# Performance work log

Hardware: AMD Instinct MI355X
Metric: run time of the kernel (lower is better)

Reference implementation:

```python
import jax, jax.numpy as jnp
import numpy as np

N_NODES = 50000
N_EDGES = 800000
HID = 128
EDGE_DIM = 4
LAYERS = 4
MAX_Z = 100
NUM_GRAPHS = 512


def setup_inputs() -> dict:
    key = jax.random.key(0)
    ks = jax.random.split(key, 16)
    s = lambda k, shape, fan_in: jax.random.normal(k, shape, jnp.float32) / np.sqrt(fan_in)
    inp = {
        "z": jax.random.randint(ks[0], (N_NODES,), 0, MAX_Z + 1),
        "edge_index": jax.random.randint(ks[1], (2, N_EDGES), 0, N_NODES),
        "edge_attr": jax.random.normal(ks[2], (N_EDGES, EDGE_DIM), jnp.float32),
        "batch": jnp.sort(jax.random.randint(ks[3], (N_NODES,), 0, NUM_GRAPHS)),
        "emb": jax.random.normal(ks[4], (MAX_Z + 1, HID), jnp.float32),
        # stacked per-layer params; Linear stored as [in, out]
        "ew1": s(ks[5], (LAYERS, 2 * HID + EDGE_DIM, HID), 2 * HID + EDGE_DIM),
        "eb1": jnp.zeros((LAYERS, HID), jnp.float32),
        "ew2": s(ks[6], (LAYERS, HID, HID), HID),
        "eb2": jnp.zeros((LAYERS, HID), jnp.float32),
        "nw": s(ks[7], (LAYERS, 2 * HID, HID), 2 * HID),
        "nb": jnp.zeros((LAYERS, HID), jnp.float32),
        "rw1": s(ks[8], (HID, HID), HID),
        "rb1": jnp.zeros((HID,), jnp.float32),
        "rw2": s(ks[9], (HID, 1), HID),
        "rb2": jnp.zeros((1,), jnp.float32),
    }
    return inp


def _forward(z, edge_index, edge_attr, batch,
             emb, ew1, eb1, ew2, eb2, nw, nb, rw1, rb1, rw2, rb2):
    silu = jax.nn.silu
    src, dst = edge_index[0], edge_index[1]
    x = emb[z]  # [N, H]
    for l in range(LAYERS):
        m_in = jnp.concatenate([x[src], x[dst], edge_attr], axis=-1)  # [E, 2H+ed]
        h = silu(m_in @ ew1[l] + eb1[l])
        msg = silu(h @ ew2[l] + eb2[l])  # [E, H]
        agg = jax.ops.segment_sum(msg, dst, num_segments=N_NODES)  # scatter-add
        x = silu(jnp.concatenate([x, agg], axis=-1) @ nw[l] + nb[l])
    # segment mean over graphs
    sums = jax.ops.segment_sum(x, batch, num_segments=NUM_GRAPHS)
    counts = jnp.clip(jax.ops.segment_sum(jnp.ones((x.shape[0],), x.dtype), batch,
                                          num_segments=NUM_GRAPHS), 1.0)[:, None]
    g = sums / counts  # [G, H]
    pred = (silu(g @ rw1 + rb1) @ rw2 + rb2)[:, 0]  # [G]
    return pred


def reference(z, edge_index, edge_attr, batch,
              emb, ew1, eb1, ew2, eb2, nw, nb, rw1, rb1, rw2, rb2):
    return _forward(z, edge_index, edge_attr, batch,
                    emb, ew1, eb1, ew2, eb2, nw, nb, rw1, rb1, rw2, rb2)
```

## Files before the change

kernel.cpp:

```cpp
#include <hip/hip_runtime.h>
#include <math.h>

#define HID  128
#define EDIM 4

typedef unsigned short u16;
typedef u16    us8   __attribute__((ext_vector_type(8)));
typedef __bf16 bf16x8 __attribute__((ext_vector_type(8)));
typedef float  f32x4 __attribute__((ext_vector_type(4)));

__device__ __forceinline__ float silu_f(float v) {
    return v * __builtin_amdgcn_rcpf(1.0f + __expf(-v));
}
__device__ __forceinline__ u16 f2bf(float f) {
    unsigned u = __float_as_uint(f);
    unsigned r = u + 0x7fffu + ((u >> 16) & 1u);
    return (u16)(r >> 16);
}
__device__ __forceinline__ u16 f2bf_fast(float f) {
    return (u16)((__float_as_uint(f) + 0x8000u) >> 16);
}
__device__ __forceinline__ unsigned pack_bf2(float a, float b) {
    return ((__float_as_uint(a) + 0x8000u) >> 16) |
           ((__float_as_uint(b) + 0x8000u) & 0xffff0000u);
}
__device__ __forceinline__ float bf2f(u16 s) {
    return __uint_as_float(((unsigned)s) << 16);
}
__device__ __forceinline__ bf16x8 as_bf(us8 v) {
    return __builtin_bit_cast(bf16x8, v);
}

__device__ __forceinline__ void wfrag_gen(const float* __restrict__ w,
        u16* __restrict__ out, int KT, int Kdata, int Kstride,
        int split, int jump, int idx) {
    int lane = idx & 63;
    int f    = (idx >> 6) % (KT * 8);
    int l    = idx / (64 * KT * 8);
    int kt = f >> 3, nt = f & 7;
    int n  = nt * 16 + (lane & 15);
    int k0 = kt * 32 + ((lane >> 4) * 8);
    us8 v;
    #pragma unroll
    for (int j = 0; j < 8; ++j) {
        int k = k0 + j;
        int row = k + (k >= split ? jump : 0);
        v[j] = (row < Kdata) ? f2bf(w[((size_t)l * Kstride + row) * HID + n]) : (u16)0;
    }
    *(us8*)&out[((size_t)(l * KT * 8 + f) * 64 + lane) * 8] = v;
}

#define T1A (4 * 5 * 8 * 64)
#define T1B (4 * 4 * 8 * 64)
#define T2  (4 * 4 * 8 * 64)
#define T3  (4 * 8 * 8 * 64)

__global__ __launch_bounds__(256) void setup_kernel(
        const float* __restrict__ ew1, const float* __restrict__ ew2,
        const float* __restrict__ nw,
        u16* __restrict__ w1af, u16* __restrict__ w1bf,
        u16* __restrict__ w2f, u16* __restrict__ nwf,
        int* __restrict__ cnt, int* __restrict__ cursor,
        float* __restrict__ sums, float* __restrict__ cnts_g, int N, int G) {
    const int BIG = 1 << 30;
    int idx = blockIdx.x * 256 + threadIdx.x;
    if (idx < T1A) { wfrag_gen(ew1, w1af, 5, 260, 260, 128, 128, idx); return; }
    idx -= T1A;
    if (idx < T1B) { wfrag_gen(ew1, w1bf, 4, 260, 260, 0, 128, idx); return; }
    idx -= T1B;
    if (idx < T2) { wfrag_gen(ew2, w2f, 4, 128, 128, BIG, 0, idx); return; }
    idx -= T2;
    if (idx < T3) { wfrag_gen(nw, nwf, 8, 256, 256, BIG, 0, idx); return; }
    idx -= T3;
    if (idx < N) { cnt[idx] = 0; return; }
    idx -= N;
    if (idx < N) { cursor[idx] = 0; return; }
    idx -= N;
    if (idx < G * HID) { sums[idx] = 0.f; return; }
    idx -= G * HID;
    if (idx < G) { cnts_g[idx] = 0.f; return; }
}

__global__ __launch_bounds__(256) void hist_kernel(const int* __restrict__ dst,
        int* __restrict__ cnt, int E) {
    int e = blockIdx.x * 256 + threadIdx.x;
    if (e < E) atomicAdd(&cnt[dst[e]], 1);
}

__global__ __launch_bounds__(1024) void scan_kernel(const int* __restrict__ cnt,
        int* __restrict__ rowptr, int n) {
    __shared__ int s[1024];
    const int t = threadIdx.x;
    const int chunk = (n + 1023) >> 10;
    int lo = t * chunk, hi = lo + chunk;
    if (lo > n) lo = n;
    if (hi > n) hi = n;
    int sum = 0;
    for (int i = lo; i < hi; ++i) sum += cnt[i];
    s[t] = sum;
    __syncthreads();
    for (int off = 1; off < 1024; off <<= 1) {
        int v = (t >= off) ? s[t - off] : 0;
        __syncthreads();
        s[t] += v;
        __syncthreads();
    }
    int run = s[t] - sum;
    for (int i = lo; i < hi; ++i) { rowptr[i] = run; run += cnt[i]; }
    if (t == 1023) rowptr[n] = run;
}

__global__ __launch_bounds__(256) void scatter_kernel(const int* __restrict__ src,
        const int* __restrict__ dst, const float* __restrict__ ea,
        const int* __restrict__ rowptr, int* __restrict__ cursor,
        int* __restrict__ srcS, int* __restrict__ dstS, u16* __restrict__ eaS, int E) {
    int e = blockIdx.x * 256 + threadIdx.x;
    if (e >= E) return;
    int d = dst[e];
    int p = rowptr[d] + atomicAdd(&cursor[d], 1);
    srcS[p] = src[e];
    dstS[p] = d;
    const float* q = &ea[(size_t)e * EDIM];
    ushort4 v;
    v.x = f2bf(q[0]); v.y = f2bf(q[1]); v.z = f2bf(q[2]); v.w = f2bf(q[3]);
    *(ushort4*)&eaS[(size_t)p * 4] = v;
}

__global__ __launch_bounds__(HID) void embed_kernel(const int* __restrict__ z,
        const float* __restrict__ emb, u16* __restrict__ xb,
        float* __restrict__ agg, const int* __restrict__ batch,
        float* __restrict__ counts, int n) {
    int i = blockIdx.x;
    if (i >= n) return;
    int t = threadIdx.x;
    xb[(size_t)i * HID + t] = f2bf(emb[(size_t)z[i] * HID + t]);
    agg[(size_t)i * HID + t] = 0.f;
    if (t == 0) unsafeAtomicAdd(&counts[batch[i]], 1.0f);
}

__global__ __launch_bounds__(256) void y_kernel(
        const u16* __restrict__ xb, const u16* __restrict__ w1bf,
        float* __restrict__ Y, int n) {
    const int t    = threadIdx.x;
    const int i0   = blockIdx.x * 32;
    const int wv   = t >> 6, lane = t & 63;
    const int lrow = lane & 15;
    const int kq   = lane >> 4;
    const int kq8  = kq * 8;

    int iN[2];
    #pragma unroll
    for (int mt = 0; mt < 2; ++mt) {
        int i = i0 + mt * 16 + lrow; if (i >= n) i = n - 1;
        iN[mt] = i;
    }
    f32x4 acc[2][2];
    #pragma unroll
    for (int mt = 0; mt < 2; ++mt)
        #pragma unroll
        for (int nt = 0; nt < 2; ++nt)
            acc[mt][nt] = (f32x4){0.f, 0.f, 0.f, 0.f};

    #pragma unroll
    for (int kt = 0; kt < 4; ++kt) {
        bf16x8 w0 = *(const bf16x8*)&w1bf[((size_t)(kt * 8 + wv * 2 + 0) * 64 + lane) * 8];
        bf16x8 w1 = *(const bf16x8*)&w1bf[((size_t)(kt * 8 + wv * 2 + 1) * 64 + lane) * 8];
        #pragma unroll
        for (int mt = 0; mt < 2; ++mt) {
            bf16x8 a = as_bf(*(const us8*)&xb[(size_t)iN[mt] * HID + kt * 32 + kq8]);
            acc[mt][0] = __builtin_amdgcn_mfma_f32_16x16x32_bf16(w0, a, acc[mt][0], 0, 0, 0);
            acc[mt][1] = __builtin_amdgcn_mfma_f32_16x16x32_bf16(w1, a, acc[mt][1], 0, 0, 0);
        }
    }
    #pragma unroll
    for (int mt = 0; mt < 2; ++mt) {
        int node = i0 + mt * 16 + lrow;
        if (node < n) {
            #pragma unroll
            for (int nt = 0; nt < 2; ++nt)
                *(f32x4*)&Y[(size_t)node * HID + (wv * 2 + nt) * 16 + kq * 4] = acc[mt][nt];
        }
    }
}

__global__ __launch_bounds__(512, 8) void edge_mfma(
        const u16* __restrict__ xin, const int* __restrict__ srcS,
        const int* __restrict__ dstS, const u16* __restrict__ eaS,
        const u16* __restrict__ w1af, const float* __restrict__ b1,
        const u16* __restrict__ w2f, const float* __restrict__ b2,
        const float* __restrict__ Y,
        float* __restrict__ agg, int nE) {
    __shared__ __align__(16) char smem[64 * 132 * 4];
    __shared__ __align__(16) int dsh[64];
    u16*   A = (u16*)smem;
    u16*   H = (u16*)smem;
    float* M = (float*)smem;

    const int t    = threadIdx.x;
    const int e0   = blockIdx.x * 64;
    const int wv   = t >> 6, lane = t & 63;
    const int lrow = lane & 15;
    const int kq   = lane >> 4;
    const int kq8  = kq * 8;
    const int rq   = kq * 4;
    const int h    = wv >> 2;
    const int p    = wv & 3;

    #pragma unroll
    for (int it = 0; it < 2; ++it) {
        int slot = it * 512 + t;
        int row = slot >> 4, ch = slot & 15;
        int e = e0 + row; if (e >= nE) e = nE - 1;
        int node = srcS[e];
        us8 v = *(const us8*)&xin[(size_t)node * HID + ch * 8];
        *(us8*)&A[row * 168 + ch * 8] = v;
    }
    if (t < 64) {
        int e = e0 + t;
        bool valid = e < nE; if (!valid) e = nE - 1;
        dsh[t] = valid ? dstS[e] : -1;
        ushort4 q = *(const ushort4*)&eaS[(size_t)e * 4];
        int base = t * 168 + 128;
        us8 z8 = (us8){0, 0, 0, 0, 0, 0, 0, 0};
        *(us8*)&A[base + 8]  = z8;
        *(us8*)&A[base + 16] = z8;
        *(us8*)&A[base + 24] = z8;
        A[base + 0] = q.x; A[base + 1] = q.y; A[base + 2] = q.z; A[base + 3] = q.w;
        A[base + 4] = 0;   A[base + 5] = 0;   A[base + 6] = 0;   A[base + 7] = 0;
    }
    __syncthreads();

    f32x4 acc[2][2];
    #pragma unroll
    for (int mt = 0; mt < 2; ++mt) {
        int edge = (h * 2 + mt) * 16 + lrow;
        int d = dsh[edge]; if (d < 0) d = 0;
        #pragma unroll
        for (int nt = 0; nt < 2; ++nt) {
            f32x4 bv = *(const f32x4*)&b1[(p * 2 + nt) * 16 + rq];
            f32x4 yv = *(const f32x4*)&Y[(size_t)d * HID + (p * 2 + nt) * 16 + rq];
            acc[mt][nt] = bv + yv;
        }
    }
    #pragma unroll
    for (int kt = 0; kt < 5; ++kt) {
        bf16x8 w0 = *(const bf16x8*)&w1af[((size_t)(kt * 8 + p * 2 + 0) * 64 + lane) * 8];
        bf16x8 w1 = *(const bf16x8*)&w1af[((size_t)(kt * 8 + p * 2 + 1) * 64 + lane) * 8];
        #pragma unroll
        for (int mt = 0; mt < 2; ++mt) {
            bf16x8 a = *(const bf16x8*)&A[((h * 2 + mt) * 16 + lrow) * 168 + kt * 32 + kq8];
            acc[mt][0] = __builtin_amdgcn_mfma_f32_16x16x32_bf16(w0, a, acc[mt][0], 0, 0, 0);
            acc[mt][1] = __builtin_amdgcn_mfma_f32_16x16x32_bf16(w1, a, acc[mt][1], 0, 0, 0);
        }
    }
    __syncthreads();

    #pragma unroll
    for (int mt = 0; mt < 2; ++mt)
        #pragma unroll
        for (int nt = 0; nt < 2; ++nt) {
            uint2 hv;
            hv.x = pack_bf2(silu_f(acc[mt][nt][0]), silu_f(acc[mt][nt][1]));
            hv.y = pack_bf2(silu_f(acc[mt][nt][2]), silu_f(acc[mt][nt][3]));
            int edge = (h * 2 + mt) * 16 + lrow;
            *(uint2*)&H[edge * 136 + (p * 2 + nt) * 16 + rq] = hv;
        }
    __syncthreads();

    f32x4 acc2[2][2];
    #pragma unroll
    for (int nt = 0; nt < 2; ++nt) {
        f32x4 bv = *(const f32x4*)&b2[(p * 2 + nt) * 16 + rq];
        acc2[0][nt] = bv; acc2[1][nt] = bv;
    }
    #pragma unroll
    for (int kt = 0; kt < 4; ++kt) {
        bf16x8 w0 = *(const bf16x8*)&w2f[((size_t)(kt * 8 + p * 2 + 0) * 64 + lane) * 8];
        bf16x8 w1 = *(const bf16x8*)&w2f[((size_t)(kt * 8 + p * 2 + 1) * 64 + lane) * 8];
        #pragma unroll
        for (int mt = 0; mt < 2; ++mt) {
            bf16x8 a = *(const bf16x8*)&H[((h * 2 + mt) * 16 + lrow) * 136 + kt * 32 + kq8];
            acc2[mt][0] = __builtin_amdgcn_mfma_f32_16x16x32_bf16(w0, a, acc2[mt][0], 0, 0, 0);
            acc2[mt][1] = __builtin_amdgcn_mfma_f32_16x16x32_bf16(w1, a, acc2[mt][1], 0, 0, 0);
        }
    }
    __syncthreads();

    #pragma unroll
    for (int mt = 0; mt < 2; ++mt)
        #pragma unroll
        for (int nt = 0; nt < 2; ++nt) {
            f32x4 mv;
            #pragma unroll
            for (int r = 0; r < 4; ++r) mv[r] = silu_f(acc2[mt][nt][r]);
            int edge = (h * 2 + mt) * 16 + lrow;
            *(f32x4*)&M[edge * 132 + (p * 2 + nt) * 16 + rq] = mv;
        }

    {
        int col = p * 32 + (lane & 31);
        int r0  = h * 32 + (lane >> 5) * 16;
        int4 da = *(const int4*)&dsh[r0];
        int4 db = *(const int4*)&dsh[r0 + 4];
        int4 dc = *(const int4*)&dsh[r0 + 8];
        int4 dd = *(const int4*)&dsh[r0 + 12];
        int ds_[16] = {da.x, da.y, da.z, da.w, db.x, db.y, db.z, db.w,
                       dc.x, dc.y, dc.z, dc.w, dd.x, dd.y, dd.z, dd.w};
        float run = 0.f;
        int   cur = ds_[0];
        #pragma unroll
        for (int i = 0; i < 16; ++i) {
            run += M[(r0 + i) * 132 + col];
            int nxt = (i == 15) ? -2 : ds_[i + 1];
            if (cur != nxt) {
                if (cur >= 0)
                    unsafeAtomicAdd(&agg[(size_t)cur * HID + col], run);
                run = 0.f; cur = nxt;
            }
        }
    }
}

__global__ __launch_bounds__(256) void node_mfma(
        u16* __restrict__ xb, float* __restrict__ agg,
        const u16* __restrict__ nwf, const float* __restrict__ nb,
        const int* __restrict__ batch, float* __restrict__ sums,
        int last, int n) {
    const int t    = threadIdx.x;
    const int i0   = blockIdx.x * 32;
    const int wv   = t >> 6, lane = t & 63;
    const int lrow = lane & 15;
    const int kq   = lane >> 4;
    const int kq8  = kq * 8;
    const int rq   = kq * 4;

    int iN[2];
    #pragma unroll
    for (int mt = 0; mt < 2; ++mt) {
        int i = i0 + mt * 16 + lrow; if (i >= n) i = n - 1;
        iN[mt] = i;
    }

    f32x4 acc[2][2];
    {
        float bias0 = nb[wv * 32 + lrow], bias1 = nb[wv * 32 + 16 + lrow];
        #pragma unroll
        for (int mt = 0; mt < 2; ++mt)
            #pragma unroll
            for (int r = 0; r < 4; ++r) {
                acc[mt][0][r] = bias0; acc[mt][1][r] = bias1;
            }
    }
    #pragma unroll
    for (int kt = 0; kt < 4; ++kt) {
        bf16x8 w0 = *(const bf16x8*)&nwf[((size_t)(kt * 8 + wv * 2 + 0) * 64 + lane) * 8];
        bf16x8 w1 = *(const bf16x8*)&nwf[((size_t)(kt * 8 + wv * 2 + 1) * 64 + lane) * 8];
        #pragma unroll
        for (int mt = 0; mt < 2; ++mt) {
            bf16x8 a = as_bf(*(const us8*)&xb[(size_t)iN[mt] * HID + kt * 32 + kq8]);
            acc[mt][0] = __builtin_amdgcn_mfma_f32_16x16x32_bf16(a, w0, acc[mt][0], 0, 0, 0);
            acc[mt][1] = __builtin_amdgcn_mfma_f32_16x16x32_bf16(a, w1, acc[mt][1], 0, 0, 0);
        }
    }
    #pragma unroll
    for (int kt = 4; kt < 8; ++kt) {
        bf16x8 w0 = *(const bf16x8*)&nwf[((size_t)(kt * 8 + wv * 2 + 0) * 64 + lane) * 8];
        bf16x8 w1 = *(const bf16x8*)&nwf[((size_t)(kt * 8 + wv * 2 + 1) * 64 + lane) * 8];
        #pragma unroll
        for (int mt = 0; mt < 2; ++mt) {
            const float* pa = &agg[(size_t)iN[mt] * HID + (kt - 4) * 32 + kq8];
            float4 f0 = *(const float4*)pa;
            float4 f1 = *(const float4*)(pa + 4);
            us8 av;
            av[0] = f2bf_fast(f0.x); av[1] = f2bf_fast(f0.y);
            av[2] = f2bf_fast(f0.z); av[3] = f2bf_fast(f0.w);
            av[4] = f2bf_fast(f1.x); av[5] = f2bf_fast(f1.y);
            av[6] = f2bf_fast(f1.z); av[7] = f2bf_fast(f1.w);
            bf16x8 a = as_bf(av);
            acc[mt][0] = __builtin_amdgcn_mfma_f32_16x16x32_bf16(a, w0, acc[mt][0], 0, 0, 0);
            acc[mt][1] = __builtin_amdgcn_mfma_f32_16x16x32_bf16(a, w1, acc[mt][1], 0, 0, 0);
        }
    }

    if (!last) {
        __syncthreads();
        const float4 z4 = make_float4(0.f, 0.f, 0.f, 0.f);
        #pragma unroll
        for (int kt = 0; kt < 4; ++kt)
            #pragma unroll
            for (int mt = 0; mt < 2; ++mt) {
                float* pa = &agg[(size_t)iN[mt] * HID + kt * 32 + kq8];
                *(float4*)pa = z4; *(float4*)(pa + 4) = z4;
            }
        #pragma unroll
        for (int mt = 0; mt < 2; ++mt)
            #pragma unroll
            for (int nt2 = 0; nt2 < 2; ++nt2)
                #pragma unroll
                for (int r = 0; r < 4; ++r) {
                    int i = i0 + mt * 16 + rq + r;
                    if (i < n)
                        xb[(size_t)i * HID + wv * 32 + nt2 * 16 + lrow] =
                            f2bf_fast(silu_f(acc[mt][nt2][r]));
                }
    } else {
        #pragma unroll
        for (int mt = 0; mt < 2; ++mt)
            #pragma unroll
            for (int nt2 = 0; nt2 < 2; ++nt2)
                #pragma unroll
                for (int r = 0; r < 4; ++r) {
                    int i = i0 + mt * 16 + rq + r;
                    if (i < n) {
                        int b = batch[i];
                        unsafeAtomicAdd(&sums[(size_t)b * HID + wv * 32 + nt2 * 16 + lrow],
                                        silu_f(acc[mt][nt2][r]));
                    }
                }
    }
}

__global__ __launch_bounds__(HID) void readout_kernel(
        const float* __restrict__ sums, const float* __restrict__ counts,
        const float* __restrict__ rw1, const float* __restrict__ rb1,
        const float* __restrict__ rw2, const float* __restrict__ rb2,
        float* __restrict__ pred) {
    __shared__ float gv[HID];
    __shared__ float hv[HID];
    const int g = blockIdx.x;
    const int t = threadIdx.x;
    float c = counts[g];
    if (c < 1.0f) c = 1.0f;
    gv[t] = sums[(size_t)g * HID + t] / c;
    __syncthreads();
    float acc = rb1[t];
    for (int k4 = 0; k4 < 32; ++k4) {
        float4 mv = *(const float4*)&gv[k4 * 4];
        #pragma unroll
        for (int j = 0; j < 4; ++j)
            acc += ((const float*)&mv)[j] * rw1[(size_t)(k4 * 4 + j) * HID + t];
    }
    hv[t] = silu_f(acc) * rw2[t];
    __syncthreads();
    for (int s = HID / 2; s > 0; s >>= 1) {
        if (t < s) hv[t] += hv[t + s];
        __syncthreads();
    }
    if (t == 0) pred[g] = hv[0] + rb2[0];
}

extern "C" void kernel_launch(void* const* d_in, const int* in_sizes, int n_in,
                              void* d_out, int out_size, void* d_ws, size_t ws_size,
                              hipStream_t stream) {
    const int*   z          = (const int*)d_in[0];
    const int*   edge_index = (const int*)d_in[1];
    const float* edge_attr  = (const float*)d_in[2];
    const int*   batch      = (const int*)d_in[3];
    const float* emb        = (const float*)d_in[4];
    const float* ew1        = (const float*)d_in[5];
    const float* eb1        = (const float*)d_in[6];
    const float* ew2        = (const float*)d_in[7];
    const float* eb2        = (const float*)d_in[8];
    const float* nw         = (const float*)d_in[9];
    const float* nb         = (const float*)d_in[10];
    const float* rw1        = (const float*)d_in[11];
    const float* rb1        = (const float*)d_in[12];
    const float* rw2        = (const float*)d_in[13];
    const float* rb2        = (const float*)d_in[14];
    float* pred = (float*)d_out;

    const int N = in_sizes[0];
    const int E = in_sizes[1] / 2;
    const int G = out_size;
    const int* srcI = edge_index;
    const int* dstI = edge_index + E;

    char* base = (char*)d_ws;
    size_t off = 0;
    auto carve = [&](size_t bytes) -> char* {
        char* p = base + off;
        off = (off + bytes + 255) & ~(size_t)255;
        return p;
    };
    float* agg    = (float*)carve((size_t)N * HID * sizeof(float));
    float* sums   = (float*)carve((size_t)G * HID * sizeof(float));
    float* cnts_g = (float*)carve((size_t)G * sizeof(float));
    u16*   xb     = (u16*)carve((size_t)N * HID * sizeof(u16));
    float* Y      = (float*)carve((size_t)N * HID * sizeof(float));
    int*   srcS   = (int*)carve((size_t)(E + 64) * sizeof(int));
    int*   dstS   = (int*)carve((size_t)(E + 64) * sizeof(int));
    u16*   eaS    = (u16*)carve((size_t)(E + 64) * 4 * sizeof(u16));
    int*   rowptr = (int*)carve((size_t)(N + 1) * sizeof(int));
    int*   cursor = (int*)carve((size_t)N * sizeof(int));
    int*   cnt    = (int*)carve((size_t)N * sizeof(int));
    u16*   w1af   = (u16*)carve((size_t)4 * 40 * 512 * sizeof(u16));
    u16*   w1bf   = (u16*)carve((size_t)4 * 32 * 512 * sizeof(u16));
    u16*   w2f    = (u16*)carve((size_t)4 * 32 * 512 * sizeof(u16));
    u16*   nwf    = (u16*)carve((size_t)4 * 64 * 512 * sizeof(u16));

    {
        long long total = (long long)T1A + T1B + T2 + T3 + 2LL * N + (long long)G * HID + G;
        int blocks = (int)((total + 255) / 256);
        setup_kernel<<<blocks, 256, 0, stream>>>(ew1, ew2, nw, w1af, w1bf, w2f, nwf,
                                                 cnt, cursor, sums, cnts_g, N, G);
    }

    hist_kernel<<<(E + 255) / 256, 256, 0, stream>>>(dstI, cnt, E);
    scan_kernel<<<1, 1024, 0, stream>>>(cnt, rowptr, N);
    scatter_kernel<<<(E + 255) / 256, 256, 0, stream>>>(
        srcI, dstI, edge_attr, rowptr, cursor, srcS, dstS, eaS, E);

    embed_kernel<<<N, HID, 0, stream>>>(z, emb, xb, agg, batch, cnts_g, N);

    for (int l = 0; l < 4; ++l) {
        y_kernel<<<(N + 31) / 32, 256, 0, stream>>>(
            xb, w1bf + (size_t)l * 32 * 512, Y, N);
        edge_mfma<<<(E + 63) / 64, 512, 0, stream>>>(
            xb, srcS, dstS, eaS,
            w1af + (size_t)l * 40 * 512, eb1 + (size_t)l * HID,
            w2f + (size_t)l * 32 * 512, eb2 + (size_t)l * HID,
            Y, agg, E);
        node_mfma<<<(N + 31) / 32, 256, 0, stream>>>(
            xb, agg, nwf + (size_t)l * 64 * 512, nb + (size_t)l * HID,
            batch, sums, (l == 3) ? 1 : 0, N);
    }

    readout_kernel<<<G, HID, 0, stream>>>(sums, cnts_g, rw1, rb1, rw2, rb2, pred);
}
```

Baseline: 1.127 ms.

## Fuse edge, node and next-layer projection into one dst-partitioned kernel

Each layer now runs as a single kernel in which every block owns 32 destination nodes. The block walks that node range's CSR edge tiles and sums messages into shared memory (aggL), so the global fp32 agg buffer, its zeroing and its global atomics are gone. After the edge tiles, the same block runs the node update and the next layer's Y projection, with x ping-ponged between two buffers. The cost is far fewer blocks, each doing a variable number of serial tiles, which can cause load imbalance. The extra shared memory may also lower occupancy.

```diff
diff --git a/kernel.cpp b/kernel.cpp
--- a/kernel.cpp
+++ b/kernel.cpp
@@ -128,13 +128,11 @@
 
 __global__ __launch_bounds__(HID) void embed_kernel(const int* __restrict__ z,
         const float* __restrict__ emb, u16* __restrict__ xb,
-        float* __restrict__ agg, const int* __restrict__ batch,
-        float* __restrict__ counts, int n) {
+        const int* __restrict__ batch, float* __restrict__ counts, int n) {
     int i = blockIdx.x;
     if (i >= n) return;
     int t = threadIdx.x;
     xb[(size_t)i * HID + t] = f2bf(emb[(size_t)z[i] * HID + t]);
-    agg[(size_t)i * HID + t] = 0.f;
     if (t == 0) unsafeAtomicAdd(&counts[batch[i]], 1.0f);
 }
 
@@ -183,21 +181,25 @@
     }
 }
 
-__global__ __launch_bounds__(512, 8) void edge_mfma(
-        const u16* __restrict__ xin, const int* __restrict__ srcS,
-        const int* __restrict__ dstS, const u16* __restrict__ eaS,
+__global__ __launch_bounds__(512, 6) void fused_layer(
+        const u16* __restrict__ xin, u16* __restrict__ xout,
+        const int* __restrict__ srcS, const int* __restrict__ dstS,
+        const u16* __restrict__ eaS, const int* __restrict__ rowptr,
         const u16* __restrict__ w1af, const float* __restrict__ b1,
         const u16* __restrict__ w2f, const float* __restrict__ b2,
-        const float* __restrict__ Y,
-        float* __restrict__ agg, int nE) {
+        float* __restrict__ Y, const u16* __restrict__ w1bf_nxt,
+        const u16* __restrict__ nwf, const float* __restrict__ nb,
+        const int* __restrict__ batch, float* __restrict__ sums,
+        int last, int N) {
     __shared__ __align__(16) char smem[64 * 132 * 4];
     __shared__ __align__(16) int dsh[64];
-    u16*   A = (u16*)smem;
-    u16*   H = (u16*)smem;
-    float* M = (float*)smem;
+    __shared__ __align__(16) float aggL[32 * HID];
+    u16*   A   = (u16*)smem;
+    u16*   H   = (u16*)smem;
+    float* M   = (float*)smem;
+    u16*   xnS = (u16*)smem;
 
     const int t    = threadIdx.x;
-    const int e0   = blockIdx.x * 64;
     const int wv   = t >> 6, lane = t & 63;
     const int lrow = lane & 15;
     const int kq   = lane >> 4;
@@ -206,217 +208,210 @@
     const int h    = wv >> 2;
     const int p    = wv & 3;
 
-    #pragma unroll
-    for (int it = 0; it < 2; ++it) {
-        int slot = it * 512 + t;
-        int row = slot >> 4, ch = slot & 15;
-        int e = e0 + row; if (e >= nE) e = nE - 1;
-        int node = srcS[e];
-        us8 v = *(const us8*)&xin[(size_t)node * HID + ch * 8];
-        *(us8*)&A[row * 168 + ch * 8] = v;
-    }
-    if (t < 64) {
-        int e = e0 + t;
-        bool valid = e < nE; if (!valid) e = nE - 1;
-        dsh[t] = valid ? dstS[e] : -1;
-        ushort4 q = *(const ushort4*)&eaS[(size_t)e * 4];
-        int base = t * 168 + 128;
-        us8 z8 = (us8){0, 0, 0, 0, 0, 0, 0, 0};
-        *(us8*)&A[base + 8]  = z8;
-        *(us8*)&A[base + 16] = z8;
-        *(us8*)&A[base + 24] = z8;
-        A[base + 0] = q.x; A[base + 1] = q.y; A[base + 2] = q.z; A[base + 3] = q.w;
-        A[base + 4] = 0;   A[base + 5] = 0;   A[base + 6] = 0;   A[base + 7] = 0;
+    const int n0  = blockIdx.x * 32;
+    int nhi = n0 + 32; if (nhi > N) nhi = N;
+    const int rs = rowptr[n0];
+    const int re = rowptr[nhi];
+    const int ntiles = (re - rs + 63) >> 6;
+
+    #pragma unroll
+    for (int i = 0; i < 2; ++i)
+        ((f32x4*)aggL)[i * 512 + t] = (f32x4){0.f, 0.f, 0.f, 0.f};
+
+    for (int tile = 0; tile < ntiles; ++tile) {
+        const int e0 = rs + tile * 64;
+        __syncthreads();
+
+        #pragma unroll
+        for (int it = 0; it < 2; ++it) {
+            int slot = it * 512 + t;
+            int row = slot >> 4, ch = slot & 15;
+            int e = e0 + row; if (e >= re) e = re - 1;
+            int node = srcS[e];
+            us8 v = *(const us8*)&xin[(size_t)node * HID + ch * 8];
+            *(us8*)&A[row * 168 + ch * 8] = v;
+        }
+        if (t < 64) {
+            int e = e0 + t;
+            bool valid = e < re; if (!valid) e = re - 1;
+            dsh[t] = valid ? (dstS[e] - n0) : -1;
+            ushort4 q = *(const ushort4*)&eaS[(size_t)e * 4];
+            int base = t * 168 + 128;
+            us8 z8 = (us8){0, 0, 0, 0, 0, 0, 0, 0};
+            *(us8*)&A[base + 8]  = z8;
+            *(us8*)&A[base + 16] = z8;
+            *(us8*)&A[base + 24] = z8;
+            A[base + 0] = q.x; A[base + 1] = q.y; A[base + 2] = q.z; A[base + 3] = q.w;
+            A[base + 4] = 0;   A[base + 5] = 0;   A[base + 6] = 0;   A[base + 7] = 0;
+        }
+        __syncthreads();
+
+        f32x4 acc[2][2];
+        #pragma unroll
+        for (int mt = 0; mt < 2; ++mt) {
+            int edge = (h * 2 + mt) * 16 + lrow;
+            int d = dsh[edge]; if (d < 0) d = 0;
+            #pragma unroll
+            for (int nt = 0; nt < 2; ++nt) {
+                f32x4 bv = *(const f32x4*)&b1[(p * 2 + nt) * 16 + rq];
+                f32x4 yv = *(const f32x4*)&Y[(size_t)(n0 + d) * HID + (p * 2 + nt) * 16 + rq];
+                acc[mt][nt] = bv + yv;
+            }
+        }
+        #pragma unroll
+        for (int kt = 0; kt < 5; ++kt) {
+            bf16x8 w0 = *(const bf16x8*)&w1af[((size_t)(kt * 8 + p * 2 + 0) * 64 + lane) * 8];
+            bf16x8 w1 = *(const bf16x8*)&w1af[((size_t)(kt * 8 + p * 2 + 1) * 64 + lane) * 8];
+            #pragma unroll
+            for (int mt = 0; mt < 2; ++mt) {
+                bf16x8 a = *(const bf16x8*)&A[((h * 2 + mt) * 16 + lrow) * 168 + kt * 32 + kq8];
+                acc[mt][0] = __builtin_amdgcn_mfma_f32_16x16x32_bf16(w0, a, acc[mt][0], 0, 0, 0);
+                acc[mt][1] = __builtin_amdgcn_mfma_f32_16x16x32_bf16(w1, a, acc[mt][1], 0, 0, 0);
+            }
+        }
+        __syncthreads();
+
+        #pragma unroll
+        for (int mt = 0; mt < 2; ++mt)
+            #pragma unroll
+            for (int nt = 0; nt < 2; ++nt) {
+                uint2 hv;
+                hv.x = pack_bf2(silu_f(acc[mt][nt][0]), silu_f(acc[mt][nt][1]));
+                hv.y = pack_bf2(silu_f(acc[mt][nt][2]), silu_f(acc[mt][nt][3]));
+                int edge = (h * 2 + mt) * 16 + lrow;
+                *(uint2*)&H[edge * 136 + (p * 2 + nt) * 16 + rq] = hv;
+            }
+        __syncthreads();
+
+        f32x4 acc2[2][2];
+        #pragma unroll
+        for (int nt = 0; nt < 2; ++nt) {
+            f32x4 bv = *(const f32x4*)&b2[(p * 2 + nt) * 16 + rq];
+            acc2[0][nt] = bv; acc2[1][nt] = bv;
+        }
+        #pragma unroll
+        for (int kt = 0; kt < 4; ++kt) {
+            bf16x8 w0 = *(const bf16x8*)&w2f[((size_t)(kt * 8 + p * 2 + 0) * 64 + lane) * 8];
+            bf16x8 w1 = *(const bf16x8*)&w2f[((size_t)(kt * 8 + p * 2 + 1) * 64 + lane) * 8];
+            #pragma unroll
+            for (int mt = 0; mt < 2; ++mt) {
+                bf16x8 a = *(const bf16x8*)&H[((h * 2 + mt) * 16 + lrow) * 136 + kt * 32 + kq8];
+                acc2[mt][0] = __builtin_amdgcn_mfma_f32_16x16x32_bf16(w0, a, acc2[mt][0], 0, 0, 0);
+                acc2[mt][1] = __builtin_amdgcn_mfma_f32_16x16x32_bf16(w1, a, acc2[mt][1], 0, 0, 0);
+            }
+        }
+        __syncthreads();
+
+        #pragma unroll
+        for (int mt = 0; mt < 2; ++mt)
+            #pragma unroll
+            for (int nt = 0; nt < 2; ++nt) {
+                f32x4 mv;
+                #pragma unroll
+                for (int r = 0; r < 4; ++r) mv[r] = silu_f(acc2[mt][nt][r]);
+                int edge = (h * 2 + mt) * 16 + lrow;
+                *(f32x4*)&M[edge * 132 + (p * 2 + nt) * 16 + rq] = mv;
+            }
+
+        {
+            int col = p * 32 + (lane & 31);
+            int r0  = h * 32 + (lane >> 5) * 16;
+            int4 da = *(const int4*)&dsh[r0];
+            int4 db = *(const int4*)&dsh[r0 + 4];
+            int4 dc = *(const int4*)&dsh[r0 + 8];
+            int4 dd = *(const int4*)&dsh[r0 + 12];
+            int ds_[16] = {da.x, da.y, da.z, da.w, db.x, db.y, db.z, db.w,
+                           dc.x, dc.y, dc.z, dc.w, dd.x, dd.y, dd.z, dd.w};
+            float run = 0.f;
+            int   cur = ds_[0];
+            #pragma unroll
+            for (int i = 0; i < 16; ++i) {
+                run += M[(r0 + i) * 132 + col];
+                int nxt = (i == 15) ? -2 : ds_[i + 1];
+                if (cur != nxt) {
+                    if (cur >= 0)
+                        atomicAdd(&aggL[cur * HID + col], run);
+                    run = 0.f; cur = nxt;
+                }
+            }
+        }
     }
     __syncthreads();
 
-    f32x4 acc[2][2];
-    #pragma unroll
-    for (int mt = 0; mt < 2; ++mt) {
-        int edge = (h * 2 + mt) * 16 + lrow;
-        int d = dsh[edge]; if (d < 0) d = 0;
-        #pragma unroll
-        for (int nt = 0; nt < 2; ++nt) {
-            f32x4 bv = *(const f32x4*)&b1[(p * 2 + nt) * 16 + rq];
-            f32x4 yv = *(const f32x4*)&Y[(size_t)d * HID + (p * 2 + nt) * 16 + rq];
-            acc[mt][nt] = bv + yv;
-        }
-    }
-    #pragma unroll
-    for (int kt = 0; kt < 5; ++kt) {
-        bf16x8 w0 = *(const bf16x8*)&w1af[((size_t)(kt * 8 + p * 2 + 0) * 64 + lane) * 8];
-        bf16x8 w1 = *(const bf16x8*)&w1af[((size_t)(kt * 8 + p * 2 + 1) * 64 + lane) * 8];
-        #pragma unroll
-        for (int mt = 0; mt < 2; ++mt) {
-            bf16x8 a = *(const bf16x8*)&A[((h * 2 + mt) * 16 + lrow) * 168 + kt * 32 + kq8];
-            acc[mt][0] = __builtin_amdgcn_mfma_f32_16x16x32_bf16(w0, a, acc[mt][0], 0, 0, 0);
-            acc[mt][1] = __builtin_amdgcn_mfma_f32_16x16x32_bf16(w1, a, acc[mt][1], 0, 0, 0);
-        }
-    }
-    __syncthreads();
-
+    f32x4 accN[2];
     #pragma unroll
     for (int mt = 0; mt < 2; ++mt)
-        #pragma unroll
-        for (int nt = 0; nt < 2; ++nt) {
-            uint2 hv;
-            hv.x = pack_bf2(silu_f(acc[mt][nt][0]), silu_f(acc[mt][nt][1]));
-            hv.y = pack_bf2(silu_f(acc[mt][nt][2]), silu_f(acc[mt][nt][3]));
-            int edge = (h * 2 + mt) * 16 + lrow;
-            *(uint2*)&H[edge * 136 + (p * 2 + nt) * 16 + rq] = hv;
-        }
-    __syncthreads();
-
-    f32x4 acc2[2][2];
-    #pragma unroll
-    for (int nt = 0; nt < 2; ++nt) {
-        f32x4 bv = *(const f32x4*)&b2[(p * 2 + nt) * 16 + rq];
-        acc2[0][nt] = bv; acc2[1][nt] = bv;
-    }
+        accN[mt] = *(const f32x4*)&nb[wv * 16 + rq];
     #pragma unroll
     for (int kt = 0; kt < 4; ++kt) {
-        bf16x8 w0 = *(const bf16x8*)&w2f[((size_t)(kt * 8 + p * 2 + 0) * 64 + lane) * 8];
-        bf16x8 w1 = *(const bf16x8*)&w2f[((size_t)(kt * 8 + p * 2 + 1) * 64 + lane) * 8];
-        #pragma unroll
-        for (int mt = 0; mt < 2; ++mt) {
-            bf16x8 a = *(const bf16x8*)&H[((h * 2 + mt) * 16 + lrow) * 136 + kt * 32 + kq8];
-            acc2[mt][0] = __builtin_amdgcn_mfma_f32_16x16x32_bf16(w0, a, acc2[mt][0], 0, 0, 0);
-            acc2[mt][1] = __builtin_amdgcn_mfma_f32_16x16x32_bf16(w1, a, acc2[mt][1], 0, 0, 0);
-        }
-    }
-    __syncthreads();
-
-    #pragma unroll
-    for (int mt = 0; mt < 2; ++mt)
-        #pragma unroll
-        for (int nt = 0; nt < 2; ++nt) {
-            f32x4 mv;
-            #pragma unroll
-            for (int r = 0; r < 4; ++r) mv[r] = silu_f(acc2[mt][nt][r]);
-            int edge = (h * 2 + mt) * 16 + lrow;
-            *(f32x4*)&M[edge * 132 + (p * 2 + nt) * 16 + rq] = mv;
-        }
-
-    {
-        int col = p * 32 + (lane & 31);
-        int r0  = h * 32 + (lane >> 5) * 16;
-        int4 da = *(const int4*)&dsh[r0];
-        int4 db = *(const int4*)&dsh[r0 + 4];
-        int4 dc = *(const int4*)&dsh[r0 + 8];
-        int4 dd = *(const int4*)&dsh[r0 + 12];
-        int ds_[16] = {da.x, da.y, da.z, da.w, db.x, db.y, db.z, db.w,
-                       dc.x, dc.y, dc.z, dc.w, dd.x, dd.y, dd.z, dd.w};
-        float run = 0.f;
-        int   cur = ds_[0];
-        #pragma unroll
-        for (int i = 0; i < 16; ++i) {
-            run += M[(r0 + i) * 132 + col];
-            int nxt = (i == 15) ? -2 : ds_[i + 1];
-            if (cur != nxt) {
-                if (cur >= 0)
-                    unsafeAtomicAdd(&agg[(size_t)cur * HID + col], run);
-                run = 0.f; cur = nxt;
-            }
-        }
-    }
-}
-
-__global__ __launch_bounds__(256) void node_mfma(
-        u16* __restrict__ xb, float* __restrict__ agg,
-        const u16* __restrict__ nwf, const float* __restrict__ nb,
-        const int* __restrict__ batch, float* __restrict__ sums,
-        int last, int n) {
-    const int t    = threadIdx.x;
-    const int i0   = blockIdx.x * 32;
-    const int wv   = t >> 6, lane = t & 63;
-    const int lrow = lane & 15;
-    const int kq   = lane >> 4;
-    const int kq8  = kq * 8;
-    const int rq   = kq * 4;
-
-    int iN[2];
-    #pragma unroll
-    for (int mt = 0; mt < 2; ++mt) {
-        int i = i0 + mt * 16 + lrow; if (i >= n) i = n - 1;
-        iN[mt] = i;
-    }
-
-    f32x4 acc[2][2];
-    {
-        float bias0 = nb[wv * 32 + lrow], bias1 = nb[wv * 32 + 16 + lrow];
-        #pragma unroll
-        for (int mt = 0; mt < 2; ++mt)
-            #pragma unroll
-            for (int r = 0; r < 4; ++r) {
-                acc[mt][0][r] = bias0; acc[mt][1][r] = bias1;
-            }
-    }
-    #pragma unroll
-    for (int kt = 0; kt < 4; ++kt) {
-        bf16x8 w0 = *(const bf16x8*)&nwf[((size_t)(kt * 8 + wv * 2 + 0) * 64 + lane) * 8];
-        bf16x8 w1 = *(const bf16x8*)&nwf[((size_t)(kt * 8 + wv * 2 + 1) * 64 + lane) * 8];
-        #pragma unroll
-        for (int mt = 0; mt < 2; ++mt) {
-            bf16x8 a = as_bf(*(const us8*)&xb[(size_t)iN[mt] * HID + kt * 32 + kq8]);
-            acc[mt][0] = __builtin_amdgcn_mfma_f32_16x16x32_bf16(a, w0, acc[mt][0], 0, 0, 0);
-            acc[mt][1] = __builtin_amdgcn_mfma_f32_16x16x32_bf16(a, w1, acc[mt][1], 0, 0, 0);
+        bf16x8 w = *(const bf16x8*)&nwf[((size_t)(kt * 8 + wv) * 64 + lane) * 8];
+        #pragma unroll
+        for (int mt = 0; mt < 2; ++mt) {
+            int nd = n0 + mt * 16 + lrow; if (nd >= N) nd = N - 1;
+            bf16x8 a = as_bf(*(const us8*)&xin[(size_t)nd * HID + kt * 32 + kq8]);
+            accN[mt] = __builtin_amdgcn_mfma_f32_16x16x32_bf16(w, a, accN[mt], 0, 0, 0);
         }
     }
     #pragma unroll
     for (int kt = 4; kt < 8; ++kt) {
-        bf16x8 w0 = *(const bf16x8*)&nwf[((size_t)(kt * 8 + wv * 2 + 0) * 64 + lane) * 8];
-        bf16x8 w1 = *(const bf16x8*)&nwf[((size_t)(kt * 8 + wv * 2 + 1) * 64 + lane) * 8];
-        #pragma unroll
-        for (int mt = 0; mt < 2; ++mt) {
-            const float* pa = &agg[(size_t)iN[mt] * HID + (kt - 4) * 32 + kq8];
-            float4 f0 = *(const float4*)pa;
-            float4 f1 = *(const float4*)(pa + 4);
+        bf16x8 w = *(const bf16x8*)&nwf[((size_t)(kt * 8 + wv) * 64 + lane) * 8];
+        #pragma unroll
+        for (int mt = 0; mt < 2; ++mt) {
+            const float* pa = &aggL[(mt * 16 + lrow) * HID + (kt - 4) * 32 + kq8];
+            f32x4 f0 = *(const f32x4*)pa;
+            f32x4 f1 = *(const f32x4*)(pa + 4);
             us8 av;
-            av[0] = f2bf_fast(f0.x); av[1] = f2bf_fast(f0.y);
-            av[2] = f2bf_fast(f0.z); av[3] = f2bf_fast(f0.w);
-            av[4] = f2bf_fast(f1.x); av[5] = f2bf_fast(f1.y);
-            av[6] = f2bf_fast(f1.z); av[7] = f2bf_fast(f1.w);
-            bf16x8 a = as_bf(av);
-            acc[mt][0] = __builtin_amdgcn_mfma_f32_16x16x32_bf16(a, w0, acc[mt][0], 0, 0, 0);
-            acc[mt][1] = __builtin_amdgcn_mfma_f32_16x16x32_bf16(a, w1, acc[mt][1], 0, 0, 0);
+            av[0] = f2bf_fast(f0[0]); av[1] = f2bf_fast(f0[1]);
+            av[2] = f2bf_fast(f0[2]); av[3] = f2bf_fast(f0[3]);
+            av[4] = f2bf_fast(f1[0]); av[5] = f2bf_fast(f1[1]);
+            av[6] = f2bf_fast(f1[2]); av[7] = f2bf_fast(f1[3]);
+            accN[mt] = __builtin_amdgcn_mfma_f32_16x16x32_bf16(w, as_bf(av), accN[mt], 0, 0, 0);
         }
     }
 
     if (!last) {
-        __syncthreads();
-        const float4 z4 = make_float4(0.f, 0.f, 0.f, 0.f);
-        #pragma unroll
-        for (int kt = 0; kt < 4; ++kt)
+        #pragma unroll
+        for (int mt = 0; mt < 2; ++mt) {
+            uint2 xv;
+            xv.x = pack_bf2(silu_f(accN[mt][0]), silu_f(accN[mt][1]));
+            xv.y = pack_bf2(silu_f(accN[mt][2]), silu_f(accN[mt][3]));
+            int node = mt * 16 + lrow;
+            *(uint2*)&xnS[node * HID + wv * 16 + rq] = xv;
+            if (n0 + node < N)
+                *(uint2*)&xout[(size_t)(n0 + node) * HID + wv * 16 + rq] = xv;
+        }
+        __syncthreads();
+
+        f32x4 accY[2];
+        accY[0] = (f32x4){0.f, 0.f, 0.f, 0.f};
+        accY[1] = (f32x4){0.f, 0.f, 0.f, 0.f};
+        #pragma unroll
+        for (int kt = 0; kt < 4; ++kt) {
+            bf16x8 w = *(const bf16x8*)&w1bf_nxt[((size_t)(kt * 8 + wv) * 64 + lane) * 8];
             #pragma unroll
             for (int mt = 0; mt < 2; ++mt) {
-                float* pa = &agg[(size_t)iN[mt] * HID + kt * 32 + kq8];
-                *(float4*)pa = z4; *(float4*)(pa + 4) = z4;
-            }
-        #pragma unroll
-        for (int mt = 0; mt < 2; ++mt)
-            #pragma unroll
-            for (int nt2 = 0; nt2 < 2; ++nt2)
+                bf16x8 a = as_bf(*(const us8*)&xnS[(mt * 16 + lrow) * HID + kt * 32 + kq8]);
+                accY[mt] = __builtin_amdgcn_mfma_f32_16x16x32_bf16(w, a, accY[mt], 0, 0, 0);
+            }
+        }
+        #pragma unroll
+        for (int mt = 0; mt < 2; ++mt) {
+            int node = mt * 16 + lrow;
+            if (n0 + node < N)
+                *(f32x4*)&Y[(size_t)(n0 + node) * HID + wv * 16 + rq] = accY[mt];
+        }
+    } else {
+        #pragma unroll
+        for (int mt = 0; mt < 2; ++mt) {
+            int node = mt * 16 + lrow;
+            if (n0 + node < N) {
+                int b = batch[n0 + node];
                 #pragma unroll
-                for (int r = 0; r < 4; ++r) {
-                    int i = i0 + mt * 16 + rq + r;
-                    if (i < n)
-                        xb[(size_t)i * HID + wv * 32 + nt2 * 16 + lrow] =
-                            f2bf_fast(silu_f(acc[mt][nt2][r]));
-                }
-    } else {
-        #pragma unroll
-        for (int mt = 0; mt < 2; ++mt)
-            #pragma unroll
-            for (int nt2 = 0; nt2 < 2; ++nt2)
-                #pragma unroll
-                for (int r = 0; r < 4; ++r) {
-                    int i = i0 + mt * 16 + rq + r;
-                    if (i < n) {
-                        int b = batch[i];
-                        unsafeAtomicAdd(&sums[(size_t)b * HID + wv * 32 + nt2 * 16 + lrow],
-                                        silu_f(acc[mt][nt2][r]));
-                    }
-                }
+                for (int r = 0; r < 4; ++r)
+                    unsafeAtomicAdd(&sums[(size_t)b * HID + wv * 16 + rq + r],
+                                    silu_f(accN[mt][r]));
+            }
+        }
     }
 }
 
@@ -482,10 +477,10 @@
         off = (off + bytes + 255) & ~(size_t)255;
         return p;
     };
-    float* agg    = (float*)carve((size_t)N * HID * sizeof(float));
     float* sums   = (float*)carve((size_t)G * HID * sizeof(float));
     float* cnts_g = (float*)carve((size_t)G * sizeof(float));
-    u16*   xb     = (u16*)carve((size_t)N * HID * sizeof(u16));
+    u16*   xbA    = (u16*)carve((size_t)N * HID * sizeof(u16));
+    u16*   xbB    = (u16*)carve((size_t)N * HID * sizeof(u16));
     float* Y      = (float*)carve((size_t)N * HID * sizeof(float));
     int*   srcS   = (int*)carve((size_t)(E + 64) * sizeof(int));
     int*   dstS   = (int*)carve((size_t)(E + 64) * sizeof(int));
@@ -510,18 +505,21 @@
     scatter_kernel<<<(E + 255) / 256, 256, 0, stream>>>(
         srcI, dstI, edge_attr, rowptr, cursor, srcS, dstS, eaS, E);
 
-    embed_kernel<<<N, HID, 0, stream>>>(z, emb, xb, agg, batch, cnts_g, N);
-
+    embed_kernel<<<N, HID, 0, stream>>>(z, emb, xbA, batch, cnts_g, N);
+
+    y_kernel<<<(N + 31) / 32, 256, 0, stream>>>(xbA, w1bf, Y, N);
+
+    const int nblk = (N + 31) / 32;
     for (int l = 0; l < 4; ++l) {
-        y_kernel<<<(N + 31) / 32, 256, 0, stream>>>(
-            xb, w1bf + (size_t)l * 32 * 512, Y, N);
-        edge_mfma<<<(E + 63) / 64, 512, 0, stream>>>(
-            xb, srcS, dstS, eaS,
+        const u16* xi = (l & 1) ? xbB : xbA;
+        u16*       xo = (l & 1) ? xbA : xbB;
+        const u16* w1b_nxt = w1bf + (size_t)((l + 1) & 3) * 32 * 512;
+        fused_layer<<<nblk, 512, 0, stream>>>(
+            xi, xo, srcS, dstS, eaS, rowptr,
             w1af + (size_t)l * 40 * 512, eb1 + (size_t)l * HID,
             w2f + (size_t)l * 32 * 512, eb2 + (size_t)l * HID,
-            Y, agg, E);
-        node_mfma<<<(N + 31) / 32, 256, 0, stream>>>(
-            xb, agg, nwf + (size_t)l * 64 * 512, nb + (size_t)l * HID,
+            Y, w1b_nxt,
+            nwf + (size_t)l * 64 * 512, nb + (size_t)l * HID,
             batch, sums, (l == 3) ? 1 : 0, N);
     }
 
```

After: 2.330 ms. 107% more time.

## Fuse next-layer Y projection into node kernel and drop edge kernel barriers

Applied to the files above, without the earlier changes.

The per-node projection of x for the next layer (Y) is now computed inside node_mfma from freshly produced x staged in shared memory, removing separate y_kernel launches and a global re-read of x. The node GEMM operand order is swapped so outputs are row-contiguous for vectorized stores. In edge_mfma, H gets its own shared buffer so two block barriers can be removed. This costs extra shared memory per block, which may reduce occupancy.

```diff
diff --git a/kernel.cpp b/kernel.cpp
--- a/kernel.cpp
+++ b/kernel.cpp
@@ -190,11 +190,12 @@
         const u16* __restrict__ w2f, const float* __restrict__ b2,
         const float* __restrict__ Y,
         float* __restrict__ agg, int nE) {
-    __shared__ __align__(16) char smem[64 * 132 * 4];
+    __shared__ __align__(16) char smemM[64 * 132 * 4];
+    __shared__ __align__(16) char smemH[64 * 136 * 2];
     __shared__ __align__(16) int dsh[64];
-    u16*   A = (u16*)smem;
-    u16*   H = (u16*)smem;
-    float* M = (float*)smem;
+    u16*   A = (u16*)smemM;
+    float* M = (float*)smemM;
+    u16*   H = (u16*)smemH;
 
     const int t    = threadIdx.x;
     const int e0   = blockIdx.x * 64;
@@ -253,7 +254,6 @@
             acc[mt][1] = __builtin_amdgcn_mfma_f32_16x16x32_bf16(w1, a, acc[mt][1], 0, 0, 0);
         }
     }
-    __syncthreads();
 
     #pragma unroll
     for (int mt = 0; mt < 2; ++mt)
@@ -284,7 +284,6 @@
             acc2[mt][1] = __builtin_amdgcn_mfma_f32_16x16x32_bf16(w1, a, acc2[mt][1], 0, 0, 0);
         }
     }
-    __syncthreads();
 
     #pragma unroll
     for (int mt = 0; mt < 2; ++mt)
@@ -325,7 +324,9 @@
         u16* __restrict__ xb, float* __restrict__ agg,
         const u16* __restrict__ nwf, const float* __restrict__ nb,
         const int* __restrict__ batch, float* __restrict__ sums,
+        float* __restrict__ Y, const u16* __restrict__ w1bf_nxt,
         int last, int n) {
+    __shared__ __align__(16) u16 xnS[32 * HID];
     const int t    = threadIdx.x;
     const int i0   = blockIdx.x * 32;
     const int wv   = t >> 6, lane = t & 63;
@@ -342,15 +343,12 @@
     }
 
     f32x4 acc[2][2];
-    {
-        float bias0 = nb[wv * 32 + lrow], bias1 = nb[wv * 32 + 16 + lrow];
-        #pragma unroll
-        for (int mt = 0; mt < 2; ++mt)
-            #pragma unroll
-            for (int r = 0; r < 4; ++r) {
-                acc[mt][0][r] = bias0; acc[mt][1][r] = bias1;
-            }
-    }
+    #pragma unroll
+    for (int mt = 0; mt < 2; ++mt)
+        #pragma unroll
+        for (int nt = 0; nt < 2; ++nt)
+            acc[mt][nt] = *(const f32x4*)&nb[(wv * 2 + nt) * 16 + rq];
+
     #pragma unroll
     for (int kt = 0; kt < 4; ++kt) {
         bf16x8 w0 = *(const bf16x8*)&nwf[((size_t)(kt * 8 + wv * 2 + 0) * 64 + lane) * 8];
@@ -358,8 +356,8 @@
         #pragma unroll
         for (int mt = 0; mt < 2; ++mt) {
             bf16x8 a = as_bf(*(const us8*)&xb[(size_t)iN[mt] * HID + kt * 32 + kq8]);
-            acc[mt][0] = __builtin_amdgcn_mfma_f32_16x16x32_bf16(a, w0, acc[mt][0], 0, 0, 0);
-            acc[mt][1] = __builtin_amdgcn_mfma_f32_16x16x32_bf16(a, w1, acc[mt][1], 0, 0, 0);
+            acc[mt][0] = __builtin_amdgcn_mfma_f32_16x16x32_bf16(w0, a, acc[mt][0], 0, 0, 0);
+            acc[mt][1] = __builtin_amdgcn_mfma_f32_16x16x32_bf16(w1, a, acc[mt][1], 0, 0, 0);
         }
     }
     #pragma unroll
@@ -377,8 +375,8 @@
             av[4] = f2bf_fast(f1.x); av[5] = f2bf_fast(f1.y);
             av[6] = f2bf_fast(f1.z); av[7] = f2bf_fast(f1.w);
             bf16x8 a = as_bf(av);
-            acc[mt][0] = __builtin_amdgcn_mfma_f32_16x16x32_bf16(a, w0, acc[mt][0], 0, 0, 0);
-            acc[mt][1] = __builtin_amdgcn_mfma_f32_16x16x32_bf16(a, w1, acc[mt][1], 0, 0, 0);
+            acc[mt][0] = __builtin_amdgcn_mfma_f32_16x16x32_bf16(w0, a, acc[mt][0], 0, 0, 0);
+            acc[mt][1] = __builtin_amdgcn_mfma_f32_16x16x32_bf16(w1, a, acc[mt][1], 0, 0, 0);
         }
     }
 
@@ -393,30 +391,61 @@
                 *(float4*)pa = z4; *(float4*)(pa + 4) = z4;
             }
         #pragma unroll
+        for (int mt = 0; mt < 2; ++mt) {
+            int node = mt * 16 + lrow;
+            #pragma unroll
+            for (int nt = 0; nt < 2; ++nt) {
+                uint2 xv;
+                xv.x = pack_bf2(silu_f(acc[mt][nt][0]), silu_f(acc[mt][nt][1]));
+                xv.y = pack_bf2(silu_f(acc[mt][nt][2]), silu_f(acc[mt][nt][3]));
+                *(uint2*)&xnS[node * HID + (wv * 2 + nt) * 16 + rq] = xv;
+                if (i0 + node < n)
+                    *(uint2*)&xb[(size_t)(i0 + node) * HID + (wv * 2 + nt) * 16 + rq] = xv;
+            }
+        }
+        __syncthreads();
+
+        f32x4 accY[2][2];
+        #pragma unroll
         for (int mt = 0; mt < 2; ++mt)
             #pragma unroll
-            for (int nt2 = 0; nt2 < 2; ++nt2)
+            for (int nt = 0; nt < 2; ++nt)
+                accY[mt][nt] = (f32x4){0.f, 0.f, 0.f, 0.f};
+        #pragma unroll
+        for (int kt = 0; kt < 4; ++kt) {
+            bf16x8 w0 = *(const bf16x8*)&w1bf_nxt[((size_t)(kt * 8 + wv * 2 + 0) * 64 + lane) * 8];
+            bf16x8 w1 = *(const bf16x8*)&w1bf_nxt[((size_t)(kt * 8 + wv * 2 + 1) * 64 + lane) * 8];
+            #pragma unroll
+            for (int mt = 0; mt < 2; ++mt) {
+                bf16x8 a = as_bf(*(const us8*)&xnS[(mt * 16 + lrow) * HID + kt * 32 + kq8]);
+                accY[mt][0] = __builtin_amdgcn_mfma_f32_16x16x32_bf16(w0, a, accY[mt][0], 0, 0, 0);
+                accY[mt][1] = __builtin_amdgcn_mfma_f32_16x16x32_bf16(w1, a, accY[mt][1], 0, 0, 0);
+            }
+        }
+        #pragma unroll
+        for (int mt = 0; mt < 2; ++mt) {
+            int node = mt * 16 + lrow;
+            if (i0 + node < n) {
                 #pragma unroll
-                for (int r = 0; r < 4; ++r) {
-                    int i = i0 + mt * 16 + rq + r;
-                    if (i < n)
-                        xb[(size_t)i * HID + wv * 32 + nt2 * 16 + lrow] =
-                            f2bf_fast(silu_f(acc[mt][nt2][r]));
-                }
+                for (int nt = 0; nt < 2; ++nt)
+                    *(f32x4*)&Y[(size_t)(i0 + node) * HID + (wv * 2 + nt) * 16 + rq] =
+                        accY[mt][nt];
+            }
+        }
     } else {
         #pragma unroll
-        for (int mt = 0; mt < 2; ++mt)
-            #pragma unroll
-            for (int nt2 = 0; nt2 < 2; ++nt2)
+        for (int mt = 0; mt < 2; ++mt) {
+            int node = mt * 16 + lrow;
+            if (i0 + node < n) {
+                int b = batch[i0 + node];
                 #pragma unroll
-                for (int r = 0; r < 4; ++r) {
-                    int i = i0 + mt * 16 + rq + r;
-                    if (i < n) {
-                        int b = batch[i];
-                        unsafeAtomicAdd(&sums[(size_t)b * HID + wv * 32 + nt2 * 16 + lrow],
-                                        silu_f(acc[mt][nt2][r]));
-                    }
-                }
+                for (int nt = 0; nt < 2; ++nt)
+                    #pragma unroll
+                    for (int r = 0; r < 4; ++r)
+                        unsafeAtomicAdd(&sums[(size_t)b * HID + (wv * 2 + nt) * 16 + rq + r],
+                                        silu_f(acc[mt][nt][r]));
+            }
+        }
     }
 }
 
@@ -512,17 +541,18 @@
 
     embed_kernel<<<N, HID, 0, stream>>>(z, emb, xb, agg, batch, cnts_g, N);
 
+    y_kernel<<<(N + 31) / 32, 256, 0, stream>>>(xb, w1bf, Y, N);
+
     for (int l = 0; l < 4; ++l) {
-        y_kernel<<<(N + 31) / 32, 256, 0, stream>>>(
-            xb, w1bf + (size_t)l * 32 * 512, Y, N);
         edge_mfma<<<(E + 63) / 64, 512, 0, stream>>>(
             xb, srcS, dstS, eaS,
             w1af + (size_t)l * 40 * 512, eb1 + (size_t)l * HID,
             w2f + (size_t)l * 32 * 512, eb2 + (size_t)l * HID,
             Y, agg, E);
+        const u16* w1b_nxt = w1bf + (size_t)((l + 1) & 3) * 32 * 512;
         node_mfma<<<(N + 31) / 32, 256, 0, stream>>>(
             xb, agg, nwf + (size_t)l * 64 * 512, nb + (size_t)l * HID,
-            batch, sums, (l == 3) ? 1 : 0, N);
+            batch, sums, Y, w1b_nxt, (l == 3) ? 1 : 0, N);
     }
 
     readout_kernel<<<G, HID, 0, stream>>>(sums, cnts_g, rw1, rb1, rw2, rb2, pred);
```

Result: slower. 1.499 ms (+33.0%).
